# Kernel tuning notes

Measured on AMD Instinct MI355X. Metric: run time of the kernel, lower is better.

## Reference

```python
import jax, jax.numpy as jnp
import numpy as np

# ---- module constants (from init_kwargs) ----
GRID = np.array([160, 160, 160], dtype=np.int32)
CENTER = np.array([0.0, 0.0, 0.0], dtype=np.float32)
SIZE = np.array([200.0, 200.0, 200.0], dtype=np.float32)
KERNEL_WIDTH = 3.0
N_SAMPLES = 128   # line-integral samples per LOR (ray-driven TOR approximation)
N_LORS = 50000

_CORNERS = [(dx, dy, dz) for dx in (0, 1) for dy in (0, 1) for dz in (0, 1)]


def _sample_line(lors, grid, center, size, n_samples, dtype):
    """lors: [N,6] (p1 xyz, p2 xyz). Returns base voxel idx i0 [N,S,3],
    trilinear fracs w [N,S,3], per-sample step length [N]."""
    p1, p2 = lors[:, 0:3], lors[:, 3:6]
    t = (jnp.arange(n_samples, dtype=dtype) + 0.5) / n_samples          # [S]
    pos = p1[:, None, :] + t[None, :, None] * (p2 - p1)[:, None, :]     # [N,S,3]
    step = jnp.linalg.norm(p2 - p1, axis=-1) / n_samples                # [N]
    gridf = grid.astype(np.float32)
    vsize = size / gridf
    origin = center - 0.5 * size
    f = (pos - origin) / vsize - 0.5        # continuous voxel-center coords
    f = jnp.clip(f, 0.0, gridf - 1.0)
    i0 = jnp.clip(jnp.floor(f).astype(jnp.int32), 0, grid - 2)          # [N,S,3]
    w = f - i0.astype(dtype)                                            # [N,S,3]
    return i0, w, step


def _corner_weight(w, c):
    dx, dy, dz = c
    wx = w[..., 0] if dx else 1.0 - w[..., 0]
    wy = w[..., 1] if dy else 1.0 - w[..., 1]
    wz = w[..., 2] if dz else 1.0 - w[..., 2]
    return wx * wy * wz


def projection(lors, image, grid, center, size, kernel_width):
    """Ray-driven line integrals through image. lors [N,6] -> [N]."""
    i0, w, step = _sample_line(lors, grid, center, size, N_SAMPLES, image.dtype)
    val = jnp.zeros(i0.shape[:2], image.dtype)   # [N,S]
    for c in _CORNERS:
        dx, dy, dz = c
        val = val + _corner_weight(w, c) * image[i0[..., 0] + dx,
                                                 i0[..., 1] + dy,
                                                 i0[..., 2] + dz]
    return kernel_width * step * val.sum(axis=1)  # [N]


def backprojection(image, grid, lors, center, size, line_integral, kernel_width):
    """Scatter line_integral back along the same rays -> volume like image."""
    i0, w, step = _sample_line(lors, grid, center, size, N_SAMPLES, image.dtype)
    contrib = (kernel_width * line_integral * step)[:, None]  # [N,1] -> bcast [N,S]
    bp = jnp.zeros(image.shape, image.dtype)
    for c in _CORNERS:
        dx, dy, dz = c
        bp = bp.at[i0[..., 0] + dx, i0[..., 1] + dy, i0[..., 2] + dz].add(
            _corner_weight(w, c) * contrib)
    return bp


def _tor_step(image, efficiency_map, xlors, ylors, zlors):
    imgz = image
    imgx = jnp.transpose(imgz, (2, 0, 1))
    imgy = jnp.transpose(imgz, (1, 0, 2))
    xl = jnp.transpose(xlors)  # [N,6]
    yl = jnp.transpose(ylors)
    zl = jnp.transpose(zlors)

    # z-direction (native axis order)
    pz = projection(zl, imgz, GRID, CENTER, SIZE, KERNEL_WIDTH)
    bpz = backprojection(imgz, GRID, zl, CENTER, SIZE, pz, KERNEL_WIDTH)

    # x-direction: permuted frame (y, z, x)
    gx = GRID[[1, 2, 0]]; cx = CENTER[[1, 2, 0]]; sx = SIZE[[1, 2, 0]]
    px = projection(xl, imgx, gx, cx, sx, KERNEL_WIDTH)
    bpx = backprojection(imgx, gx, xl, cx, sx, px, KERNEL_WIDTH)
    bpxt = jnp.transpose(bpx, (1, 2, 0))

    # y-direction: permuted frame (x, z, y)
    gy = GRID[[0, 2, 1]]; cy = CENTER[[0, 2, 1]]; sy = SIZE[[0, 2, 1]]
    py = projection(yl, imgy, gy, cy, sy, KERNEL_WIDTH)
    bpy = backprojection(imgy, gy, yl, cy, sy, py, KERNEL_WIDTH)
    bpyt = jnp.transpose(bpy, (1, 0, 2))

    return imgz * efficiency_map * (bpxt + bpyt + bpz)


def setup_inputs() -> dict:
    key = jax.random.key(0)
    k_img, k_eff, kx, ky, kz = jax.random.split(key, 5)
    image = jax.random.uniform(k_img, tuple(GRID), dtype=jnp.float32)
    effmap = jax.random.uniform(k_eff, tuple(GRID), dtype=jnp.float32)
    lo = jnp.asarray(np.concatenate([CENTER - 0.5 * SIZE] * 2), jnp.float32)   # [6]
    span = jnp.asarray(np.concatenate([SIZE] * 2), jnp.float32)                # [6]
    def mk(k):
        u = jax.random.uniform(k, (6, N_LORS), dtype=jnp.float32)
        return u * span[:, None] + lo[:, None]
    return {"image": image, "efficiency_map": effmap,
            "xlors": mk(kx), "ylors": mk(ky), "zlors": mk(kz)}


def reference(image, efficiency_map, xlors, ylors, zlors):
    return _tor_step(image, efficiency_map, xlors, ylors, zlors)
```

## Files before the change

kernel.cpp:

```cpp
#include <hip/hip_runtime.h>

#define NL 50000
#define NS 128
#define G 160
#define GSQ (160*160)
#define GCUBE (160*160*160)
#define NRB 196
#define NBINS (G*2)
#define ENT_CAP 11500000

struct RayParam { float4 a, b; };

__device__ __forceinline__ void lds_add(float* p, float v) {
    atomicAdd(p, v);
}

__device__ __forceinline__ float frcp(float x) {
#if __has_builtin(__builtin_amdgcn_rcpf)
    return __builtin_amdgcn_rcpf(x);
#else
    return 1.0f / x;
#endif
}

__device__ __forceinline__ void coordf(float pos, int& i, float& w) {
    float f = (pos + 100.0f) * 0.8f - 0.5f;
    f = fminf(fmaxf(f, 0.0f), 159.0f);
    int ii = (int)f; ii = ii > 158 ? 158 : ii;
    i = ii; w = f - (float)ii;
}

__device__ __forceinline__ int cnt_for(float A, float B, float rB, int p, int& slo_out) {
    const float glo = (p <= 1)   ? -1.0f  : (float)(p - 1);
    const float ghi = (p >= 158) ? 160.0f : (float)(p + 1);
    int slo, shi;
    if (B == 0.0f) {
        if (A < glo || A > ghi) { slo_out = 0; return 0; }
        slo = 0; shi = NS - 1;
    } else {
        const float t1 = (glo - A) * rB, t2 = (ghi - A) * rB;
        const float tlo = fminf(t1, t2), thi = fmaxf(t1, t2);
        float slof = ceilf (tlo * (float)NS - 0.75f);
        float shif = floorf(thi * (float)NS - 0.25f);
        slof = fminf(fmaxf(slof,  0.0f), 127.0f);
        shif = fminf(fmaxf(shif, -1.0f), 127.0f);
        slo = (int)slof; shi = (int)shif;
    }
    slo_out = slo;
    return shi - slo + 1;
}

__device__ __forceinline__ void halves_for(
    float A, float B, float rB, int p, float AR, float BR,
    int& lo0, int& n0, int& lo1, int& n1)
{
    lo0 = lo1 = 0; n0 = n1 = 0;
    int slo; const int c = cnt_for(A, B, rB, p, slo);
    if (c <= 0) return;
    const int shi = slo + c - 1;
    if (BR == 0.0f) {
        if (AR < 80.0f) { lo0 = slo; n0 = c; } else { lo1 = slo; n1 = c; }
        return;
    }
    float sstar = ((80.0f - AR) * frcp(BR)) * (float)NS - 0.5f;
    sstar = fminf(fmaxf(sstar, -300.0f), 300.0f);
    float lo0f, hi0f, lo1f, hi1f;
    if (BR > 0.0f) {
        lo0f = (float)slo;  hi0f = fminf((float)shi, floorf(sstar) + 1.0f);
        lo1f = fmaxf((float)slo, ceilf(sstar) - 1.0f);  hi1f = (float)shi;
    } else {
        lo1f = (float)slo;  hi1f = fminf((float)shi, floorf(sstar) + 1.0f);
        lo0f = fmaxf((float)slo, ceilf(sstar) - 1.0f);  hi0f = (float)shi;
    }
    lo0 = (int)lo0f; n0 = (int)hi0f - lo0 + 1; if (n0 < 0) n0 = 0;
    lo1 = (int)lo1f; n1 = (int)hi1f - lo1 + 1; if (n1 < 0) n1 = 0;
}

__device__ __forceinline__ void plane_range(float A, float B, int& plo, int& phi) {
    const float f0 = A + B * (0.5f / NS);
    const float f1 = A + B * (((float)NS - 0.5f) / NS);
    const float fmn = fminf(f0, f1), fmx = fmaxf(f0, f1);
    plo = (int)fmaxf(ceilf (fmn - 1.01f), 0.0f);
    phi = (int)fminf(floorf(fmx + 1.01f), 159.0f);
}

template<int PA, int PB, int PC, int QS, int QR, int QC>
__device__ __forceinline__ void proj_body(
    const float* __restrict__ img,
    const float* __restrict__ lors,
    float* __restrict__ contrib,
    RayParam* __restrict__ params,
    int sa, int sb, int bx)
{
    const int wave = threadIdx.x >> 6;
    const int lane = threadIdx.x & 63;
    const int lor  = bx * 4 + wave;

    const float p1x = lors[0*NL + lor];
    const float p1y = lors[1*NL + lor];
    const float p1z = lors[2*NL + lor];
    const float dxv = lors[3*NL + lor] - p1x;
    const float dyv = lors[4*NL + lor] - p1y;
    const float dzv = lors[5*NL + lor] - p1z;
    const float len  = sqrtf(dxv*dxv + dyv*dyv + dzv*dzv);
    const float step = len * (1.0f/NS);

    float2 P00[2], P01[2], P10[2], P11[2];
    float waq[2], wbq[2], wcq[2];

    #pragma unroll
    for (int q = 0; q < 2; ++q) {
        const int s = lane + q*64;
        const float t = ((float)s + 0.5f) * (1.0f/NS);
        const float pos[3] = { p1x + t*dxv, p1y + t*dyv, p1z + t*dzv };
        int ia, ib, ic; float wa, wb, wc;
        coordf(pos[PA], ia, wa);
        coordf(pos[PB], ib, wb);
        coordf(pos[PC], ic, wc);
        const float* g = img + ia*sa + ib*sb + ic;
        __builtin_memcpy(&P00[q], g,            8);
        __builtin_memcpy(&P01[q], g + sb,       8);
        __builtin_memcpy(&P10[q], g + sa,       8);
        __builtin_memcpy(&P11[q], g + sa + sb,  8);
        waq[q] = wa; wbq[q] = wb; wcq[q] = wc;
    }

    float sum = 0.0f;
    #pragma unroll
    for (int q = 0; q < 2; ++q) {
        const float wa = waq[q], wb = wbq[q], wc = wcq[q];
        const float c00 = P00[q].x + wc*(P00[q].y - P00[q].x);
        const float c01 = P01[q].x + wc*(P01[q].y - P01[q].x);
        const float c10 = P10[q].x + wc*(P10[q].y - P10[q].x);
        const float c11 = P11[q].x + wc*(P11[q].y - P11[q].x);
        const float c0  = c00 + wb*(c01 - c00);
        const float c1  = c10 + wb*(c11 - c10);
        sum += c0 + wa*(c1 - c0);
    }

    #pragma unroll
    for (int off = 32; off > 0; off >>= 1)
        sum += __shfl_xor(sum, off, 64);

    if (lane == 0) {
        const float cb = 9.0f * step * step * sum;
        contrib[lor] = cb;
        if (params) {
            const float P1v[3] = { p1x, p1y, p1z };
            const float DVv[3] = { dxv, dyv, dzv };
            float4 a, b;
            a.x = (P1v[QS] + 100.0f)*0.8f - 0.5f;  a.y = DVv[QS]*0.8f;
            a.z = (P1v[QR] + 100.0f)*0.8f - 0.5f;  a.w = DVv[QR]*0.8f;
            b.x = (P1v[QC] + 100.0f)*0.8f - 0.5f;  b.y = DVv[QC]*0.8f;
            b.z = cb;                               b.w = 0.0f;
            params[lor].a = a;
            params[lor].b = b;
        }
    }
}

__global__ __launch_bounds__(256) void proj_all(
    const float* __restrict__ img,
    const float* __restrict__ xl, const float* __restrict__ yl,
    const float* __restrict__ zl,
    float* __restrict__ cz, float* __restrict__ cx, float* __restrict__ cy,
    RayParam* __restrict__ params)
{
    const int bx = blockIdx.x;
    if (blockIdx.y == 0)
        proj_body<0,1,2, 0,1,2>(img, zl, cz, params ? params        : nullptr, GSQ, G, bx);
    else if (blockIdx.y == 1)
        proj_body<1,2,0, 1,2,0>(img, xl, cx, params ? params +   NL : nullptr, GSQ, G, bx);
    else
        proj_body<0,1,2, 1,0,2>(img, yl, cy, params ? params + 2*NL : nullptr, G, GSQ, bx);
}

__global__ __launch_bounds__(256) void bin_count(
    const RayParam* __restrict__ params, int* __restrict__ totals)
{
    const int rb = blockIdx.x, pass = blockIdx.y;
    __shared__ int cnt[NBINS];
    for (int i = threadIdx.x; i < NBINS; i += 256) cnt[i] = 0;
    __syncthreads();

    const int r = rb*256 + threadIdx.x;
    if (r < NL) {
        const float4 a = params[pass*NL + r].a;
        const float A = a.x, B = a.y, AR = a.z, BR = a.w;
        int plo, phi; plane_range(A, B, plo, phi);
        const float rB = frcp(B);
        for (int p = plo; p <= phi; ++p) {
            int lo0, n0, lo1, n1;
            halves_for(A, B, rB, p, AR, BR, lo0, n0, lo1, n1);
            if (n0 > 0) atomicAdd(&cnt[p*2    ], (n0 + 7) >> 3);
            if (n1 > 0) atomicAdd(&cnt[p*2 + 1], (n1 + 7) >> 3);
        }
    }
    __syncthreads();
    for (int i = threadIdx.x; i < NBINS; i += 256)
        if (cnt[i]) atomicAdd(&totals[i], cnt[i]);
}

__global__ __launch_bounds__(512) void scan320(
    const int* __restrict__ totals, int* __restrict__ offsets,
    int* __restrict__ cur)
{
    __shared__ int v[NBINS];
    const int tid = threadIdx.x;
    int mine = 0;
    if (tid < NBINS) { mine = totals[tid]; v[tid] = mine; }
    __syncthreads();
    for (int off = 1; off < NBINS; off <<= 1) {
        int x = 0;
        if (tid < NBINS && tid >= off) x = v[tid - off];
        __syncthreads();
        if (tid < NBINS) v[tid] += x;
        __syncthreads();
    }
    if (tid < NBINS) {
        const int excl = v[tid] - mine;
        offsets[tid] = excl;
        cur[tid]     = excl;
    }
    if (tid == 0) offsets[NBINS] = v[NBINS-1];
}

__global__ __launch_bounds__(256) void bin_write(
    const RayParam* __restrict__ params, int* __restrict__ cur,
    unsigned* __restrict__ entries)
{
    const int rb = blockIdx.x, pass = blockIdx.y;
    __shared__ int cnt[NBINS];
    __shared__ int base[NBINS];
    for (int i = threadIdx.x; i < NBINS; i += 256) cnt[i] = 0;
    __syncthreads();

    const int r = rb*256 + threadIdx.x;
    float A = 0, B = 0, AR = 0, BR = 0, rB = 0;
    int plo = 0, phi = -1;
    if (r < NL) {
        const float4 a = params[pass*NL + r].a;
        A = a.x; B = a.y; AR = a.z; BR = a.w;
        plane_range(A, B, plo, phi);
        rB = frcp(B);
        for (int p = plo; p <= phi; ++p) {
            int lo0, n0, lo1, n1;
            halves_for(A, B, rB, p, AR, BR, lo0, n0, lo1, n1);
            if (n0 > 0) atomicAdd(&cnt[p*2    ], (n0 + 7) >> 3);
            if (n1 > 0) atomicAdd(&cnt[p*2 + 1], (n1 + 7) >> 3);
        }
    }
    __syncthreads();
    for (int i = threadIdx.x; i < NBINS; i += 256) {
        const int c = cnt[i];
        base[i] = c ? atomicAdd(&cur[i], c) : 0;
    }
    __syncthreads();
    for (int i = threadIdx.x; i < NBINS; i += 256) cnt[i] = 0;
    __syncthreads();

    if (r < NL) {
        for (int p = plo; p <= phi; ++p) {
            int lo0, n0, lo1, n1;
            halves_for(A, B, rB, p, AR, BR, lo0, n0, lo1, n1);
            #pragma unroll
            for (int h = 0; h < 2; ++h) {
                const int lo = h ? lo1 : lo0;
                const int n  = h ? n1  : n0;
                if (n > 0) {
                    const int bin = p*2 + h;
                    const int ke = (n + 7) >> 3;
                    const int gb = base[bin] + atomicAdd(&cnt[bin], ke);
                    for (int e = 0; e < ke; ++e) {
                        const int s0 = lo + e*8;
                        const int nn = (n - e*8) < 8 ? (n - e*8) : 8;
                        const unsigned enc = (unsigned)r | ((unsigned)s0 << 17)
                                           | ((unsigned)(nn-1) << 24)
                                           | ((unsigned)pass << 27);
                        if (gb + e < ENT_CAP) entries[gb + e] = enc;
                    }
                }
            }
        }
    }
}

__global__ __launch_bounds__(512) void bp_half(
    const RayParam* __restrict__ params, const int* __restrict__ offsets,
    const unsigned* __restrict__ entries,
    float* __restrict__ out)
{
    __shared__ float tile[81*G];
    const int b   = blockIdx.x;
    const int c   = blockIdx.y;
    const int p   = b >> 1;
    const int h   = b & 1;
    const int tid = threadIdx.x;
    const int rowbase = 80 * h;

    for (int j = tid; j < 81*G; j += 512) tile[j] = 0.0f;
    __syncthreads();

    int s0 = offsets[b];
    int e0 = offsets[b+1];
    if (e0 > ENT_CAP) e0 = ENT_CAP;
    if (s0 > e0) s0 = e0;
    const int n  = e0 - s0;
    const int cs = s0 + (n *  c     ) / 2;
    const int ce = s0 + (n * (c + 1)) / 2;
    const int cn = ce - cs;

    const int my_s = cs + (int)(((long long)cn * tid)       >> 9);
    const int my_e = cs + (int)(((long long)cn * (tid + 1)) >> 9);

    int   pk  = -1;
    float a00 = 0.0f, a01 = 0.0f, a10 = 0.0f, a11 = 0.0f;

    unsigned enc = 0; RayParam rp;
    if (my_s < my_e) {
        enc = entries[my_s];
        rp  = params[(enc >> 27)*NL + (enc & 0x1FFFF)];
    }

    for (int e = my_s; e < my_e; ++e) {
        unsigned encN = 0;
        if (e + 1 < my_e) encN = entries[e + 1];

        const int ss = (enc >> 17) & 0x7F;
        const int nn = ((enc >> 24) & 0x7) + 1;
        const float A = rp.a.x, B = rp.a.y, AR = rp.a.z, BR = rp.a.w;
        const float AC = rp.b.x, BC = rp.b.y, cb = rp.b.z;

        for (int i = 0; i < nn; ++i) {
            const float t = ((float)(ss + i) + 0.5f) * (1.0f/NS);
            float fA = A + B*t;
            fA = fminf(fmaxf(fA, 0.0f), 159.0f);
            int ia = (int)fA; ia = ia > 158 ? 158 : ia;
            const float wa = fA - (float)ia;
            float fa;
            if (ia == p)          fa = 1.0f - wa;
            else if (ia == p - 1) fa = wa;
            else                  fa = -1.0f;

            float fR = AR + BR*t;
            fR = fminf(fmaxf(fR, 0.0f), 159.0f);
            int ib = (int)fR; ib = ib > 158 ? 158 : ib;
            const int rl = ib - rowbase;

            if (fa >= 0.0f && rl >= 0 && rl <= 79) {
                float fC = AC + BC*t;
                fC = fminf(fmaxf(fC, 0.0f), 159.0f);
                int ic = (int)fC; ic = ic > 158 ? 158 : ic;
                const float wb = fR - (float)ib;
                const float wc = fC - (float)ic;
                const float v  = fa * cb;
                const float v0 = v * (1.0f - wb), v1 = v * wb;
                const int key = rl*G + ic;
                if (key != pk) {
                    if (pk >= 0) {
                        float* q = tile + pk;
                        lds_add(q,         a00);
                        lds_add(q + 1,     a01);
                        lds_add(q + G,     a10);
                        lds_add(q + G + 1, a11);
                    }
                    pk = key;
                    a00 = 0.0f; a01 = 0.0f; a10 = 0.0f; a11 = 0.0f;
                }
                a00 += v0 * (1.0f - wc);
                a01 += v0 * wc;
                a10 += v1 * (1.0f - wc);
                a11 += v1 * wc;
            }
        }

        if (e + 1 < my_e) {
            if (((encN ^ enc) & 0x1801FFFFu) != 0u)
                rp = params[(encN >> 27)*NL + (encN & 0x1FFFF)];
        }
        enc = encN;
    }

    if (pk >= 0) {
        float* q = tile + pk;
        lds_add(q,         a00);
        lds_add(q + 1,     a01);
        lds_add(q + G,     a10);
        lds_add(q + G + 1, a11);
    }
    __syncthreads();

    const int nrows = h ? 80 : 81;
    float* dst = out + (size_t)p * GSQ + (size_t)rowbase * G;
    for (int j = tid; j < nrows*G; j += 512) {
#if __has_builtin(__builtin_amdgcn_global_atomic_fadd_f32)
        unsafeAtomicAdd(&dst[j], tile[j]);
#else
        atomicAdd(&dst[j], tile[j]);
#endif
    }
}

__global__ __launch_bounds__(256) void finalize_mul(
    const float4* __restrict__ img, const float4* __restrict__ eff,
    float4* __restrict__ out)
{
    const int i = blockIdx.x * 256 + threadIdx.x;
    const float4 a = img[i];
    const float4 e = eff[i];
    float4 o = out[i];
    o.x *= a.x * e.x;
    o.y *= a.y * e.y;
    o.z *= a.z * e.z;
    o.w *= a.w * e.w;
    out[i] = o;
}

template<int PS, int PR, int PC2>
__device__ __forceinline__ void slab_accum(
    float* __restrict__ plane,
    const float* __restrict__ lors,
    const float* __restrict__ contrib,
    int p, int wave, int lane, int nwaves)
{
    for (int base = wave*64; base < NL; base += nwaves*64) {
        const int r = base + lane;
        float A = 0.f, B = 0.f, AR = 0.f, BR = 0.f, AC = 0.f, BC = 0.f, cb = 0.f;
        int slo = 0, cnt = 0;
        if (r < NL) {
            const float q0 = lors[0*NL + r], q1 = lors[1*NL + r], q2 = lors[2*NL + r];
            const float d0 = lors[3*NL + r] - q0;
            const float d1 = lors[4*NL + r] - q1;
            const float d2 = lors[5*NL + r] - q2;
            const float P1[3] = { q0, q1, q2 };
            const float DV[3] = { d0, d1, d2 };
            A  = (P1[PS]  + 100.0f)*0.8f - 0.5f;  B  = DV[PS]*0.8f;
            AR = (P1[PR]  + 100.0f)*0.8f - 0.5f;  BR = DV[PR]*0.8f;
            AC = (P1[PC2] + 100.0f)*0.8f - 0.5f;  BC = DV[PC2]*0.8f;
            cb = contrib[r];
            const float rB = frcp(B);
            cnt = cnt_for(A, B, rB, p, slo);
            if (cnt < 0) cnt = 0;
        }

        int pref = cnt;
        #pragma unroll
        for (int off = 1; off < 64; off <<= 1) {
            const int nsh = __shfl_up(pref, off, 64);
            if (lane >= off) pref += nsh;
        }
        const int total = __shfl(pref, 63, 64);
        const int start = pref - cnt;

        for (int k0 = 0; k0 < total; k0 += 64) {
            const int k  = k0 + lane;
            const int kc = k < total ? k : total - 1;

            int j = 0;
            #pragma unroll
            for (int stp = 32; stp >= 1; stp >>= 1) {
                const int cand = j + stp;
                const int sc = __shfl(start, cand, 64);
                if (cand < 64 && sc <= kc) j = cand;
            }

            const int   sj  = __shfl(slo,   j, 64);
            const int   stj = __shfl(start, j, 64);
            const float Aj  = __shfl(A,  j, 64);
            const float Bj  = __shfl(B,  j, 64);
            const float ARj = __shfl(AR, j, 64);
            const float BRj = __shfl(BR, j, 64);
            const float ACj = __shfl(AC, j, 64);
            const float BCj = __shfl(BC, j, 64);
            const float cbj = __shfl(cb, j, 64);

            const int s = sj + (kc - stj);
            const float t = ((float)s + 0.5f) * (1.0f/NS);
            float fA = Aj + Bj * t;
            fA = fminf(fmaxf(fA, 0.0f), 159.0f);
            int ia = (int)fA; ia = ia > 158 ? 158 : ia;
            const float wa = fA - (float)ia;
            float fa;
            if (ia == p)          fa = 1.0f - wa;
            else if (ia == p - 1) fa = wa;
            else                  fa = -1.0f;

            float fR = ARj + BRj * t;
            float fC = ACj + BCj * t;
            fR = fminf(fmaxf(fR, 0.0f), 159.0f);
            fC = fminf(fmaxf(fC, 0.0f), 159.0f);
            int ib = (int)fR; ib = ib > 158 ? 158 : ib;
            int ic = (int)fC; ic = ic > 158 ? 158 : ic;
            const float wb = fR - (float)ib;
            const float wc = fC - (float)ic;

            if (k < total && fa >= 0.0f) {
                const float v  = fa * cbj;
                const float v0 = v * (1.0f - wb), v1 = v * wb;
                float* q = plane + ib*G + ic;
                lds_add(q,         v0 * (1.0f - wc));
                lds_add(q + 1,     v0 * wc);
                lds_add(q + G,     v1 * (1.0f - wc));
                lds_add(q + G + 1, v1 * wc);
            }
        }
    }
}

__global__ __launch_bounds__(1024) void bp_fused(
    const float* __restrict__ img, const float* __restrict__ eff,
    const float* __restrict__ zl, const float* __restrict__ xl,
    const float* __restrict__ yl,
    const float* __restrict__ cz, const float* __restrict__ cx,
    const float* __restrict__ cy,
    float* __restrict__ out)
{
    __shared__ float plane[GSQ];
    const int p    = blockIdx.x;
    const int tid  = threadIdx.x;
    const int wave = tid >> 6;
    const int lane = tid & 63;

    for (int j = tid; j < GSQ; j += 1024) plane[j] = 0.0f;
    __syncthreads();

    slab_accum<0,1,2>(plane, zl, cz, p, wave, lane, 16);
    slab_accum<1,2,0>(plane, xl, cx, p, wave, lane, 16);
    slab_accum<1,0,2>(plane, yl, cy, p, wave, lane, 16);

    __syncthreads();

    const int pbase = p * GSQ;
    for (int j = tid; j < GSQ; j += 1024) {
        const int idx = pbase + j;
        out[idx] = plane[j] * img[idx] * eff[idx];
    }
}

extern "C" void kernel_launch(void* const* d_in, const int* in_sizes, int n_in,
                              void* d_out, int out_size, void* d_ws, size_t ws_size,
                              hipStream_t stream) {
    const float* img = (const float*)d_in[0];
    const float* eff = (const float*)d_in[1];
    const float* xl  = (const float*)d_in[2];
    const float* yl  = (const float*)d_in[3];
    const float* zl  = (const float*)d_in[4];
    float* out = (float*)d_out;

    const size_t CONTRIB_B = (size_t)3*NL*sizeof(float);
    const size_t PARAMS_B  = (size_t)3*NL*sizeof(RayParam);
    const size_t TOT_B     = (size_t)NBINS*sizeof(int);
    const size_t OFFS_B    = (size_t)(NBINS+1)*sizeof(int);
    const size_t CUR_B     = (size_t)NBINS*sizeof(int);
    const size_t ENT_B     = (size_t)ENT_CAP*sizeof(unsigned);

    char* w = (char*)d_ws;
    float*    cz      = (float*)w;
    float*    cx      = cz + NL;
    float*    cy      = cx + NL;
    RayParam* params  = (RayParam*)(w + CONTRIB_B);
    int*      totals  = (int*)(w + CONTRIB_B + PARAMS_B);
    int*      offsets = (int*)(w + CONTRIB_B + PARAMS_B + TOT_B);
    int*      cur     = (int*)(w + CONTRIB_B + PARAMS_B + TOT_B + OFFS_B);
    unsigned* entries = (unsigned*)(w + CONTRIB_B + PARAMS_B + TOT_B + OFFS_B + CUR_B);

    const bool binned =
        ws_size >= CONTRIB_B + PARAMS_B + TOT_B + OFFS_B + CUR_B + ENT_B;

    proj_all<<<dim3(NL/4, 3), dim3(256), 0, stream>>>(
        img, xl, yl, zl, cz, cx, cy, binned ? params : nullptr);

    if (binned) {
        hipMemsetAsync(out, 0, (size_t)GCUBE * sizeof(float), stream);
        hipMemsetAsync(totals, 0, TOT_B, stream);
        bin_count<<<dim3(NRB, 3), dim3(256), 0, stream>>>(params, totals);
        scan320  <<<dim3(1),      dim3(512), 0, stream>>>(totals, offsets, cur);
        bin_write<<<dim3(NRB, 3), dim3(256), 0, stream>>>(params, cur, entries);
        bp_half  <<<dim3(NBINS,2),dim3(512), 0, stream>>>(params, offsets, entries, out);
        finalize_mul<<<dim3(GCUBE/4/256), dim3(256), 0, stream>>>(
            (const float4*)img, (const float4*)eff, (float4*)out);
    } else {
        bp_fused<<<dim3(G), dim3(1024), 0, stream>>>(
            img, eff, zl, xl, yl, cz, cx, cy, out);
    }
}
```

Before: 1.389 ms.

## Interleave backprojection entries across threads and carry shared corners between adjacent cells

Each thread now takes entries in a block-strided pattern (cs+tid, step 512) rather than a contiguous chunk, so a wavefront's entry loads are coalesced. Because neighbouring entries no longer belong to the same thread, the check that skipped reloading ray params for the same ray is gone, and params are now loaded for every entry. When the accumulator key moves by one cell in either axis, only the two corners that leave the 2x2 footprint are flushed to LDS and the two shared ones are carried over, which cuts LDS atomics. The cost is less locality per thread, so keys change more often, along with extra branching.

Measured after the change: 1.139 ms. 18.0% less time.

```diff
diff --git a/kernel.cpp b/kernel.cpp
--- a/kernel.cpp
+++ b/kernel.cpp
@@ -308,23 +308,21 @@
     const int n  = e0 - s0;
     const int cs = s0 + (n *  c     ) / 2;
     const int ce = s0 + (n * (c + 1)) / 2;
-    const int cn = ce - cs;
-
-    const int my_s = cs + (int)(((long long)cn * tid)       >> 9);
-    const int my_e = cs + (int)(((long long)cn * (tid + 1)) >> 9);
+
+    int e = cs + tid;
+    unsigned enc = 0; RayParam rp;
+    if (e < ce) {
+        enc = entries[e];
+        rp  = params[(enc >> 27)*NL + (enc & 0x1FFFF)];
+    }
 
     int   pk  = -1;
     float a00 = 0.0f, a01 = 0.0f, a10 = 0.0f, a11 = 0.0f;
 
-    unsigned enc = 0; RayParam rp;
-    if (my_s < my_e) {
-        enc = entries[my_s];
-        rp  = params[(enc >> 27)*NL + (enc & 0x1FFFF)];
-    }
-
-    for (int e = my_s; e < my_e; ++e) {
+    while (e < ce) {
+        const int en = e + 512;
         unsigned encN = 0;
-        if (e + 1 < my_e) encN = entries[e + 1];
+        if (en < ce) encN = entries[en];
 
         const int ss = (enc >> 17) & 0x7F;
         const int nn = ((enc >> 24) & 0x7) + 1;
@@ -359,13 +357,32 @@
                 if (key != pk) {
                     if (pk >= 0) {
                         float* q = tile + pk;
-                        lds_add(q,         a00);
-                        lds_add(q + 1,     a01);
-                        lds_add(q + G,     a10);
-                        lds_add(q + G + 1, a11);
+                        const int d = key - pk;
+                        if (d == 1) {
+                            lds_add(q,     a00);
+                            lds_add(q + G, a10);
+                            a00 = a01; a10 = a11; a01 = 0.0f; a11 = 0.0f;
+                        } else if (d == -1) {
+                            lds_add(q + 1,     a01);
+                            lds_add(q + G + 1, a11);
+                            a01 = a00; a11 = a10; a00 = 0.0f; a10 = 0.0f;
+                        } else if (d == G) {
+                            lds_add(q,     a00);
+                            lds_add(q + 1, a01);
+                            a00 = a10; a01 = a11; a10 = 0.0f; a11 = 0.0f;
+                        } else if (d == -G) {
+                            lds_add(q + G,     a10);
+                            lds_add(q + G + 1, a11);
+                            a10 = a00; a11 = a01; a00 = 0.0f; a01 = 0.0f;
+                        } else {
+                            lds_add(q,         a00);
+                            lds_add(q + 1,     a01);
+                            lds_add(q + G,     a10);
+                            lds_add(q + G + 1, a11);
+                            a00 = 0.0f; a01 = 0.0f; a10 = 0.0f; a11 = 0.0f;
+                        }
                     }
                     pk = key;
-                    a00 = 0.0f; a01 = 0.0f; a10 = 0.0f; a11 = 0.0f;
                 }
                 a00 += v0 * (1.0f - wc);
                 a01 += v0 * wc;
@@ -374,11 +391,9 @@
             }
         }
 
-        if (e + 1 < my_e) {
-            if (((encN ^ enc) & 0x1801FFFFu) != 0u)
-                rp = params[(encN >> 27)*NL + (encN & 0x1FFFF)];
-        }
-        enc = encN;
+        if (en < ce)
+            rp = params[(encN >> 27)*NL + (encN & 0x1FFFF)];
+        enc = encN; e = en;
     }
 
     if (pk >= 0) {
```
